# Kernel tuning notes

Hardware: AMD Instinct MI355X
Metric: run time of the kernel (lower is better)

The kernel has to match this reference:

```python
import jax, jax.numpy as jnp
import numpy as np

ORDER_WEIGHT = 1.0
RELATION_WEIGHT = 0.5

B, N, R = 32, 384, 16


def setup_inputs() -> dict:
    key = jax.random.key(0)
    k1, k2, k3, k4, k5, k6 = jax.random.split(key, 6)
    order_logits = jax.random.normal(k1, (B, N, N), dtype=jnp.float32)
    relation_logits = jax.random.normal(k2, (B, N, N, R), dtype=jnp.float32)
    reading_orders = jax.random.randint(k3, (B, N), 0, N)
    # parent_ids in [-1, N): -1 means root (no relation loss contribution)
    parent_ids = jax.random.randint(k4, (B, N), -1, N)
    # relations in [-1, R): -1 means ignored
    relations = jax.random.randint(k5, (B, N), -1, R)
    region_mask = jax.random.randint(k6, (B, N), 0, 2).astype(jnp.bool_)
    return {
        "order_logits": order_logits,
        "relation_logits": relation_logits,
        "reading_orders": reading_orders,
        "parent_ids": parent_ids,
        "relations": relations,
        "region_mask": region_mask,
    }


def reference(order_logits, relation_logits, reading_orders, parent_ids, relations, region_mask):
    b, n = reading_orders.shape
    # ---- pairwise reading-order BCE loss ----
    targets = (reading_orders[:, :, None] < reading_orders[:, None, :]).astype(order_logits.dtype)
    valid_mask = region_mask[:, :, None] & region_mask[:, None, :]
    valid_mask = valid_mask & (~jnp.eye(n, dtype=jnp.bool_))[None, :, :]
    # stable BCE-with-logits: softplus(x) - x*t
    bce = jnp.logaddexp(jnp.zeros_like(order_logits), order_logits) - order_logits * targets
    vm = valid_mask.astype(order_logits.dtype)
    order_loss = (bce * vm).sum() / jnp.maximum(valid_mask.sum(), 1).astype(order_logits.dtype)

    # ---- relation cross-entropy loss (vectorized gather) ----
    rel_valid = region_mask & (parent_ids >= 0) & (parent_ids < n) & (relations >= 0)
    p = jnp.clip(parent_ids, 0, n - 1)                       # [B, N]
    rel = jnp.clip(relations, 0, relation_logits.shape[-1] - 1)
    b_idx = jnp.arange(b)[:, None]
    i_idx = jnp.arange(n)[None, :]
    pair_logits = relation_logits[b_idx, p, i_idx]           # [B, N, R]
    ce = jax.nn.logsumexp(pair_logits, axis=-1) - jnp.take_along_axis(
        pair_logits, rel[:, :, None], axis=-1)[:, :, 0]      # [B, N]
    rv = rel_valid.astype(ce.dtype)
    relation_loss = (ce * rv).sum() / jnp.maximum(rel_valid.sum(), 1).astype(ce.dtype)

    total_loss = ORDER_WEIGHT * order_loss + RELATION_WEIGHT * relation_loss
    return total_loss, order_loss, relation_loss
```

## Files before the change

kernel.cpp:

```cpp
#include <hip/hip_runtime.h>

#define BB 32
#define NN 384
#define RR 16

__device__ __forceinline__ float softplus_f(float x) {
    return fmaxf(x, 0.0f) + log1pf(expf(-fabsf(x)));
}

__device__ __forceinline__ float blockReduceSumF(float val, float* smem) {
    #pragma unroll
    for (int off = 32; off > 0; off >>= 1) val += __shfl_down(val, off, 64);
    int lane = threadIdx.x & 63;
    int wave = threadIdx.x >> 6;
    if (lane == 0) smem[wave] = val;
    __syncthreads();
    int nw = blockDim.x >> 6;
    if (wave == 0) {
        val = (lane < nw) ? smem[lane] : 0.0f;
        #pragma unroll
        for (int off = 32; off > 0; off >>= 1) val += __shfl_down(val, off, 64);
    }
    return val;
}

__device__ __forceinline__ int blockReduceSumI(int val, int* smem) {
    #pragma unroll
    for (int off = 32; off > 0; off >>= 1) val += __shfl_down(val, off, 64);
    int lane = threadIdx.x & 63;
    int wave = threadIdx.x >> 6;
    if (lane == 0) smem[wave] = val;
    __syncthreads();
    int nw = blockDim.x >> 6;
    if (wave == 0) {
        val = (lane < nw) ? smem[lane] : 0;
        #pragma unroll
        for (int off = 32; off > 0; off >>= 1) val += __shfl_down(val, off, 64);
    }
    return val;
}

__global__ void order_loss_kernel(const float* __restrict__ order_logits,
                                  const int* __restrict__ reading_orders,
                                  const unsigned char* __restrict__ region_mask,
                                  float* __restrict__ ws) {
    const int N4 = NN / 4;
    const int total4 = BB * NN * N4;
    float sum = 0.0f;
    int cnt = 0;
    for (int idx = blockIdx.x * blockDim.x + threadIdx.x; idx < total4;
         idx += gridDim.x * blockDim.x) {
        int j4 = (idx % N4) * 4;
        int bi = idx / N4;
        int i  = bi % NN;
        int b  = bi / NN;
        if (!region_mask[bi]) continue;
        int ro_i = reading_orders[bi];
        float4 x4 = ((const float4*)order_logits)[idx];
        const int bBase = b * NN;
        #pragma unroll
        for (int k = 0; k < 4; ++k) {
            int j = j4 + k;
            float x = (&x4.x)[k];
            if (region_mask[bBase + j] && (i != j)) {
                float t = (ro_i < reading_orders[bBase + j]) ? 1.0f : 0.0f;
                sum += softplus_f(x) - x * t;
                cnt++;
            }
        }
    }
    __shared__ float sf[8];
    __shared__ int si[8];
    float bs = blockReduceSumF(sum, sf);
    int bc = blockReduceSumI(cnt, si);
    if (threadIdx.x == 0) {
        atomicAdd(&ws[0], bs);
        atomicAdd((int*)&ws[1], bc);
    }
}

__global__ void relation_loss_kernel(const float* __restrict__ relation_logits,
                                     const int* __restrict__ parent_ids,
                                     const int* __restrict__ relations,
                                     const unsigned char* __restrict__ region_mask,
                                     float* __restrict__ ws) {
    int t = blockIdx.x * blockDim.x + threadIdx.x;
    float sum = 0.0f;
    int cnt = 0;
    if (t < BB * NN) {
        int b = t / NN, i = t % NN;
        int p = parent_ids[t];
        int r = relations[t];
        if (region_mask[t] && p >= 0 && p < NN && r >= 0) {
            const float4* row =
                (const float4*)(relation_logits + ((size_t)(b * NN + p) * NN + i) * RR);
            float v[RR];
            float4 a0 = row[0], a1 = row[1], a2 = row[2], a3 = row[3];
            v[0]=a0.x; v[1]=a0.y; v[2]=a0.z; v[3]=a0.w;
            v[4]=a1.x; v[5]=a1.y; v[6]=a1.z; v[7]=a1.w;
            v[8]=a2.x; v[9]=a2.y; v[10]=a2.z; v[11]=a2.w;
            v[12]=a3.x; v[13]=a3.y; v[14]=a3.z; v[15]=a3.w;
            float m = v[0];
            #pragma unroll
            for (int k = 1; k < RR; ++k) m = fmaxf(m, v[k]);
            float s = 0.0f;
            #pragma unroll
            for (int k = 0; k < RR; ++k) s += expf(v[k] - m);
            float lse = m + logf(s);
            sum = lse - v[r];
            cnt = 1;
        }
    }
    __shared__ float sf[8];
    __shared__ int si[8];
    float bs = blockReduceSumF(sum, sf);
    int bc = blockReduceSumI(cnt, si);
    if (threadIdx.x == 0) {
        atomicAdd(&ws[2], bs);
        atomicAdd((int*)&ws[3], bc);
    }
}

__global__ void finalize_kernel(const float* __restrict__ ws, float* __restrict__ out) {
    if (threadIdx.x == 0) {
        float os = ws[0];
        int oc = ((const int*)ws)[1];
        float rs = ws[2];
        int rc = ((const int*)ws)[3];
        float order_loss = os / (float)(oc > 1 ? oc : 1);
        float rel_loss = rs / (float)(rc > 1 ? rc : 1);
        out[0] = 1.0f * order_loss + 0.5f * rel_loss;
        out[1] = order_loss;
        out[2] = rel_loss;
    }
}

extern "C" void kernel_launch(void* const* d_in, const int* in_sizes, int n_in,
                              void* d_out, int out_size, void* d_ws, size_t ws_size,
                              hipStream_t stream) {
    const float* order_logits    = (const float*)d_in[0];
    const float* relation_logits = (const float*)d_in[1];
    const int* reading_orders    = (const int*)d_in[2];
    const int* parent_ids        = (const int*)d_in[3];
    const int* relations         = (const int*)d_in[4];
    const unsigned char* region_mask = (const unsigned char*)d_in[5];
    float* out = (float*)d_out;
    float* ws  = (float*)d_ws;

    hipMemsetAsync(ws, 0, 4 * sizeof(float), stream);

    order_loss_kernel<<<1024, 256, 0, stream>>>(order_logits, reading_orders,
                                                region_mask, ws);
    relation_loss_kernel<<<(BB * NN + 255) / 256, 256, 0, stream>>>(
        relation_logits, parent_ids, relations, region_mask, ws);
    finalize_kernel<<<1, 64, 0, stream>>>(ws, out);
}
```

Baseline: 371.5 us.

## Fuse order and relation loss kernels, replace atomics with per-block partials

Merges the order-loss and relation-loss kernels into one launch. Each block now writes a float4 of partial sums and counts to workspace instead of doing global atomics, and the finalize kernel reduces all 768 partials. This drops the memset, one kernel launch and the atomic contention. The grid shrinks from 1024 to 768 blocks, which gives fewer threads for the bandwidth-bound order loop.

```diff
diff --git a/kernel.cpp b/kernel.cpp
--- a/kernel.cpp
+++ b/kernel.cpp
@@ -3,102 +3,89 @@
 #define BB 32
 #define NN 384
 #define RR 16
+#define GRID_MAIN 768
+#define BLK 256
 
 __device__ __forceinline__ float softplus_f(float x) {
     return fmaxf(x, 0.0f) + log1pf(expf(-fabsf(x)));
 }
 
-__device__ __forceinline__ float blockReduceSumF(float val, float* smem) {
+__device__ __forceinline__ void blockReduce4(float& f0, int& c0, float& f1, int& c1) {
     #pragma unroll
-    for (int off = 32; off > 0; off >>= 1) val += __shfl_down(val, off, 64);
+    for (int off = 32; off > 0; off >>= 1) {
+        f0 += __shfl_down(f0, off, 64);
+        c0 += __shfl_down(c0, off, 64);
+        f1 += __shfl_down(f1, off, 64);
+        c1 += __shfl_down(c1, off, 64);
+    }
+    __shared__ float sf0[16], sf1[16];
+    __shared__ int   sc0[16], sc1[16];
     int lane = threadIdx.x & 63;
     int wave = threadIdx.x >> 6;
-    if (lane == 0) smem[wave] = val;
+    if (lane == 0) { sf0[wave] = f0; sc0[wave] = c0; sf1[wave] = f1; sc1[wave] = c1; }
     __syncthreads();
     int nw = blockDim.x >> 6;
     if (wave == 0) {
-        val = (lane < nw) ? smem[lane] : 0.0f;
+        f0 = (lane < nw) ? sf0[lane] : 0.0f;
+        c0 = (lane < nw) ? sc0[lane] : 0;
+        f1 = (lane < nw) ? sf1[lane] : 0.0f;
+        c1 = (lane < nw) ? sc1[lane] : 0;
         #pragma unroll
-        for (int off = 32; off > 0; off >>= 1) val += __shfl_down(val, off, 64);
+        for (int off = 32; off > 0; off >>= 1) {
+            f0 += __shfl_down(f0, off, 64);
+            c0 += __shfl_down(c0, off, 64);
+            f1 += __shfl_down(f1, off, 64);
+            c1 += __shfl_down(c1, off, 64);
+        }
     }
-    return val;
 }
 
-__device__ __forceinline__ int blockReduceSumI(int val, int* smem) {
-    #pragma unroll
-    for (int off = 32; off > 0; off >>= 1) val += __shfl_down(val, off, 64);
-    int lane = threadIdx.x & 63;
-    int wave = threadIdx.x >> 6;
-    if (lane == 0) smem[wave] = val;
-    __syncthreads();
-    int nw = blockDim.x >> 6;
-    if (wave == 0) {
-        val = (lane < nw) ? smem[lane] : 0;
-        #pragma unroll
-        for (int off = 32; off > 0; off >>= 1) val += __shfl_down(val, off, 64);
-    }
-    return val;
-}
-
-__global__ void order_loss_kernel(const float* __restrict__ order_logits,
-                                  const int* __restrict__ reading_orders,
-                                  const unsigned char* __restrict__ region_mask,
-                                  float* __restrict__ ws) {
+__global__ __launch_bounds__(BLK) void main_loss_kernel(
+        const float* __restrict__ order_logits,
+        const float* __restrict__ relation_logits,
+        const int* __restrict__ reading_orders,
+        const int* __restrict__ parent_ids,
+        const int* __restrict__ relations,
+        const unsigned char* __restrict__ region_mask,
+        float4* __restrict__ ws) {
     const int N4 = NN / 4;
     const int total4 = BB * NN * N4;
-    float sum = 0.0f;
-    int cnt = 0;
-    for (int idx = blockIdx.x * blockDim.x + threadIdx.x; idx < total4;
-         idx += gridDim.x * blockDim.x) {
+    const int gid = blockIdx.x * BLK + threadIdx.x;
+
+    float oSum = 0.0f; int oCnt = 0;
+    for (int idx = gid; idx < total4; idx += GRID_MAIN * BLK) {
         int j4 = (idx % N4) * 4;
         int bi = idx / N4;
+        if (!region_mask[bi]) continue;
         int i  = bi % NN;
-        int b  = bi / NN;
-        if (!region_mask[bi]) continue;
+        int bBase = bi - i;
         int ro_i = reading_orders[bi];
         float4 x4 = ((const float4*)order_logits)[idx];
-        const int bBase = b * NN;
         #pragma unroll
         for (int k = 0; k < 4; ++k) {
             int j = j4 + k;
             float x = (&x4.x)[k];
             if (region_mask[bBase + j] && (i != j)) {
                 float t = (ro_i < reading_orders[bBase + j]) ? 1.0f : 0.0f;
-                sum += softplus_f(x) - x * t;
-                cnt++;
+                oSum += softplus_f(x) - x * t;
+                oCnt++;
             }
         }
     }
-    __shared__ float sf[8];
-    __shared__ int si[8];
-    float bs = blockReduceSumF(sum, sf);
-    int bc = blockReduceSumI(cnt, si);
-    if (threadIdx.x == 0) {
-        atomicAdd(&ws[0], bs);
-        atomicAdd((int*)&ws[1], bc);
-    }
-}
 
-__global__ void relation_loss_kernel(const float* __restrict__ relation_logits,
-                                     const int* __restrict__ parent_ids,
-                                     const int* __restrict__ relations,
-                                     const unsigned char* __restrict__ region_mask,
-                                     float* __restrict__ ws) {
-    int t = blockIdx.x * blockDim.x + threadIdx.x;
-    float sum = 0.0f;
-    int cnt = 0;
-    if (t < BB * NN) {
-        int b = t / NN, i = t % NN;
-        int p = parent_ids[t];
-        int r = relations[t];
-        if (region_mask[t] && p >= 0 && p < NN && r >= 0) {
+    float rSum = 0.0f; int rCnt = 0;
+    if (gid < BB * NN) {
+        int b = gid / NN, i = gid % NN;
+        int p = parent_ids[gid];
+        int r = relations[gid];
+        if (region_mask[gid] && p >= 0 && p < NN && r >= 0) {
             const float4* row =
                 (const float4*)(relation_logits + ((size_t)(b * NN + p) * NN + i) * RR);
             float v[RR];
             float4 a0 = row[0], a1 = row[1], a2 = row[2], a3 = row[3];
-            v[0]=a0.x; v[1]=a0.y; v[2]=a0.z; v[3]=a0.w;
-            v[4]=a1.x; v[5]=a1.y; v[6]=a1.z; v[7]=a1.w;
-            v[8]=a2.x; v[9]=a2.y; v[10]=a2.z; v[11]=a2.w;
+            v[0]=a0.x;  v[1]=a0.y;  v[2]=a0.z;  v[3]=a0.w;
+            v[4]=a1.x;  v[5]=a1.y;  v[6]=a1.z;  v[7]=a1.w;
+            v[8]=a2.x;  v[9]=a2.y;  v[10]=a2.z; v[11]=a2.w;
             v[12]=a3.x; v[13]=a3.y; v[14]=a3.z; v[15]=a3.w;
             float m = v[0];
             #pragma unroll
@@ -106,29 +93,37 @@
             float s = 0.0f;
             #pragma unroll
             for (int k = 0; k < RR; ++k) s += expf(v[k] - m);
-            float lse = m + logf(s);
-            sum = lse - v[r];
-            cnt = 1;
+            rSum = m + logf(s) - v[r];
+            rCnt = 1;
         }
     }
-    __shared__ float sf[8];
-    __shared__ int si[8];
-    float bs = blockReduceSumF(sum, sf);
-    int bc = blockReduceSumI(cnt, si);
+
+    blockReduce4(oSum, oCnt, rSum, rCnt);
     if (threadIdx.x == 0) {
-        atomicAdd(&ws[2], bs);
-        atomicAdd((int*)&ws[3], bc);
+        float4 out;
+        out.x = oSum;
+        out.y = __int_as_float(oCnt);
+        out.z = rSum;
+        out.w = __int_as_float(rCnt);
+        ws[blockIdx.x] = out;
     }
 }
 
-__global__ void finalize_kernel(const float* __restrict__ ws, float* __restrict__ out) {
+__global__ __launch_bounds__(BLK) void finalize_kernel(const float4* __restrict__ ws,
+                                                       float* __restrict__ out) {
+    float oSum = 0.0f, rSum = 0.0f;
+    int oCnt = 0, rCnt = 0;
+    for (int i = threadIdx.x; i < GRID_MAIN; i += BLK) {
+        float4 v = ws[i];
+        oSum += v.x;
+        oCnt += __float_as_int(v.y);
+        rSum += v.z;
+        rCnt += __float_as_int(v.w);
+    }
+    blockReduce4(oSum, oCnt, rSum, rCnt);
     if (threadIdx.x == 0) {
-        float os = ws[0];
-        int oc = ((const int*)ws)[1];
-        float rs = ws[2];
-        int rc = ((const int*)ws)[3];
-        float order_loss = os / (float)(oc > 1 ? oc : 1);
-        float rel_loss = rs / (float)(rc > 1 ? rc : 1);
+        float order_loss = oSum / (float)(oCnt > 1 ? oCnt : 1);
+        float rel_loss   = rSum / (float)(rCnt > 1 ? rCnt : 1);
         out[0] = 1.0f * order_loss + 0.5f * rel_loss;
         out[1] = order_loss;
         out[2] = rel_loss;
@@ -144,14 +139,11 @@
     const int* parent_ids        = (const int*)d_in[3];
     const int* relations         = (const int*)d_in[4];
     const unsigned char* region_mask = (const unsigned char*)d_in[5];
-    float* out = (float*)d_out;
-    float* ws  = (float*)d_ws;
+    float* out  = (float*)d_out;
+    float4* ws4 = (float4*)d_ws;
 
-    hipMemsetAsync(ws, 0, 4 * sizeof(float), stream);
-
-    order_loss_kernel<<<1024, 256, 0, stream>>>(order_logits, reading_orders,
-                                                region_mask, ws);
-    relation_loss_kernel<<<(BB * NN + 255) / 256, 256, 0, stream>>>(
-        relation_logits, parent_ids, relations, region_mask, ws);
-    finalize_kernel<<<1, 64, 0, stream>>>(ws, out);
+    main_loss_kernel<<<GRID_MAIN, BLK, 0, stream>>>(
+        order_logits, relation_logits, reading_orders, parent_ids, relations,
+        region_mask, ws4);
+    finalize_kernel<<<1, BLK, 0, stream>>>(ws4, out);
 }
```

Result: faster. 349.1 us (-6.0%).
